# Optimization experiments

Hardware: AMD Instinct MI355X
Metric: run time of the kernel (lower is better)

The kernel has to match this reference:

```python
import jax, jax.numpy as jnp
import numpy as np

B, S, D = 8, 512, 768
H = 12          # attention heads
E = 14          # routed experts
K = 4           # top-k experts per sequence
HID = D * 2     # expert mlp hidden (mlp_ratio=2)
SH = D * 2 * 2  # shared expert hidden (mlp_ratio * n_shared_experts)
EPS = 1e-5


def _ln(x, g, b):
    m = x.mean(-1, keepdims=True)
    v = ((x - m) ** 2).mean(-1, keepdims=True)
    return (x - m) / jnp.sqrt(v + EPS) * g + b


def _gelu(x):
    return jax.nn.gelu(x, approximate=False)


def setup_inputs() -> dict:
    key = jax.random.key(0)
    ks = jax.random.split(key, 12)
    p = lambda k, shape: jax.random.normal(k, shape, jnp.float32) * 0.02
    z = lambda *shape: jnp.zeros(shape, jnp.float32)
    return {
        "x": jax.random.normal(ks[0], (B, S, D), jnp.float32),
        "ln1_g": jnp.ones((D,), jnp.float32), "ln1_b": z(D),
        "qkv_w": p(ks[1], (D, 3 * D)),
        "proj_w": p(ks[2], (D, D)), "proj_b": z(D),
        "ln2_g": jnp.ones((D,), jnp.float32), "ln2_b": z(D),
        "router_w1": p(ks[3], (D, D)), "router_b1": z(D),
        "router_w2": p(ks[4], (D, E)), "router_b2": z(E),
        "exp_w1": p(ks[5], (E, D, HID)), "exp_b1": z(E, HID),
        "exp_w2": p(ks[6], (E, HID, D)), "exp_b2": z(E, D),
        "sh_w1": p(ks[7], (D, SH)), "sh_b1": z(SH),
        "sh_w2": p(ks[8], (SH, D)), "sh_b2": z(D),
    }


def _forward(x, ln1_g, ln1_b, qkv_w, proj_w, proj_b, ln2_g, ln2_b,
             router_w1, router_b1, router_w2, router_b2,
             exp_w1, exp_b1, exp_w2, exp_b2,
             sh_w1, sh_b1, sh_w2, sh_b2):
    dh = D // H
    scale = dh ** -0.5
    # --- attention branch ---
    h1 = _ln(x, ln1_g, ln1_b)
    qkv = (h1 @ qkv_w).reshape(B, S, 3, H, dh)
    q = jnp.moveaxis(qkv[:, :, 0], 2, 1)  # [B,H,S,dh]
    k = jnp.moveaxis(qkv[:, :, 1], 2, 1)
    v = jnp.moveaxis(qkv[:, :, 2], 2, 1)
    att = jax.nn.softmax(jnp.einsum('bhqd,bhkd->bhqk', q, k) * scale, axis=-1)
    ao = jnp.einsum('bhqk,bhkd->bqhd', att, v).reshape(B, S, D) @ proj_w + proj_b
    x2 = x + ao
    # --- MoE branch ---
    h = _ln(x2, ln2_g, ln2_b)
    seq_repr = h.mean(axis=1)                                   # [B,D]
    logits = _gelu(seq_repr @ router_w1 + router_b1) @ router_w2 + router_b2  # [B,E]
    probs = jax.nn.softmax(logits, axis=-1)
    tw, ti = jax.lax.top_k(probs, K)                            # [B,K]
    tw = jax.nn.softmax(tw, axis=-1)                            # re-normalize top-k
    w = (jax.nn.one_hot(ti, E, dtype=tw.dtype) * tw[..., None]).sum(1)  # [B,E]
    # dense all-expert compute; zero weight off the top-k replicates masked routing
    hid = _gelu(jnp.einsum('bsd,edh->ebsh', h, exp_w1) + exp_b1[:, None, None, :])
    eo = jnp.einsum('ebsh,ehd->ebsd', hid, exp_w2) + exp_b2[:, None, None, :]
    y = jnp.einsum('ebsd,be->bsd', eo, w)
    # shared experts
    y = y + _gelu(h @ sh_w1 + sh_b1) @ sh_w2 + sh_b2
    return x2 + y  # ls2 is Identity (init_values=None); aux_loss=0 in eval


def reference(x, ln1_g, ln1_b, qkv_w, proj_w, proj_b, ln2_g, ln2_b,
              router_w1, router_b1, router_w2, router_b2,
              exp_w1, exp_b1, exp_w2, exp_b2,
              sh_w1, sh_b1, sh_w2, sh_b2):
    return _forward(x, ln1_g, ln1_b, qkv_w, proj_w, proj_b, ln2_g, ln2_b,
                    router_w1, router_b1, router_w2, router_b2,
                    exp_w1, exp_b1, exp_w2, exp_b2,
                    sh_w1, sh_b1, sh_w2, sh_b2)
```

## Files before the change

### kernel.cpp

```cpp
#include <hip/hip_runtime.h>
#include <hip/hip_bf16.h>


typedef _Float16 f16x8 __attribute__((ext_vector_type(8)));
typedef float f32x4 __attribute__((ext_vector_type(4)));
typedef _Float16 f16;

__device__ __forceinline__ float gelu_fast(float x) {
  const float k2l2e = 2.f * 0.7978845608028654f * 1.4426950408889634f;
  float u = (x + 0.044715f * x * x * x) * k2l2e;
  float t = exp2f(u);
  return x * (1.f - 1.f / (t + 1.f));
}

__device__ __forceinline__ f32x4 mfma16(f16x8 a, f16x8 b, f32x4 c) {
  return __builtin_amdgcn_mfma_f32_16x16x32_f16(a, b, c, 0, 0, 0);
}

#define ASYNC_CP16(g, l)                                            \
  __builtin_amdgcn_global_load_lds(                                 \
      (const __attribute__((address_space(1))) void*)(g),           \
      (__attribute__((address_space(3))) void*)(l), 16, 0, 0)

#define GEMM_STAGE(AB, WB, LDA, LDB, koff, buf)                               \
  ASYNC_CP16(&(AB)[(long)fr * (LDA) + (koff) + fc],        &sA[(buf) * 4096 + f]);        \
  ASYNC_CP16(&(AB)[(long)(fr + 64) * (LDA) + (koff) + fc], &sA[(buf) * 4096 + f + 2048]); \
  ASYNC_CP16(&(WB)[(long)fr * (LDB) + (koff) + fc],        &sB[(buf) * 4096 + f]);        \
  ASYNC_CP16(&(WB)[(long)(fr + 64) * (LDB) + (koff) + fc], &sB[(buf) * 4096 + f + 2048]);

#define GEMM_CORE(AB, WB, LDA, LDB, KK)                                       \
  {                                                                           \
    GEMM_STAGE(AB, WB, LDA, LDB, 0, 0)                                        \
    __syncthreads();                                                          \
    int cur = 0;                                                              \
    for (int k0 = 0; k0 < (KK); k0 += 32) {                                   \
      f16x8 av[4], bv[4];                                                     \
      _Pragma("unroll")                                                       \
      for (int i = 0; i < 4; i++)                                             \
        av[i] = *(const f16x8*)&sA[cur * 4096 + (wm + i * 16 + lr) * 32 + q4 * 8]; \
      _Pragma("unroll")                                                       \
      for (int j = 0; j < 4; j++)                                             \
        bv[j] = *(const f16x8*)&sB[cur * 4096 + (wn + j * 16 + lr) * 32 + q4 * 8]; \
      if (k0 + 32 < (KK)) {                                                   \
        GEMM_STAGE(AB, WB, LDA, LDB, k0 + 32, cur ^ 1)                        \
      }                                                                       \
      _Pragma("unroll")                                                       \
      for (int i = 0; i < 4; i++)                                             \
        _Pragma("unroll")                                                     \
        for (int j = 0; j < 4; j++) acc[i][j] = mfma16(av[i], bv[j], acc[i][j]); \
      if (k0 + 32 < (KK)) __syncthreads();                                    \
      cur ^= 1;                                                               \
    }                                                                         \
  }

__global__ __launch_bounds__(256) void ln_kernel(
    const float* __restrict__ x, const float* __restrict__ g,
    const float* __restrict__ bt, f16* __restrict__ out,
    float* __restrict__ mout, float* __restrict__ rout)
{
  const int row = blockIdx.x;
  const float* xr = x + (long)row * 768;
  const int t = threadIdx.x;
  float v0 = xr[t], v1 = xr[t + 256], v2 = xr[t + 512];
  __shared__ float sb[8];
  float s = v0 + v1 + v2;
  #pragma unroll
  for (int o = 32; o > 0; o >>= 1) s += __shfl_xor(s, o, 64);
  const int w = t >> 6;
  if ((t & 63) == 0) sb[w] = s;
  __syncthreads();
  const float mean = (sb[0] + sb[1] + sb[2] + sb[3]) * (1.0f / 768.0f);
  const float d0 = v0 - mean, d1 = v1 - mean, d2 = v2 - mean;
  float q = d0 * d0 + d1 * d1 + d2 * d2;
  #pragma unroll
  for (int o = 32; o > 0; o >>= 1) q += __shfl_xor(q, o, 64);
  if ((t & 63) == 0) sb[4 + w] = q;
  __syncthreads();
  const float var = (sb[4] + sb[5] + sb[6] + sb[7]) * (1.0f / 768.0f);
  const float rstd = rsqrtf(var + 1e-5f);
  f16* orow = out + (long)row * 768;
  orow[t]       = (f16)(d0 * rstd * g[t]       + bt[t]);
  orow[t + 256] = (f16)(d1 * rstd * g[t + 256] + bt[t + 256]);
  orow[t + 512] = (f16)(d2 * rstd * g[t + 512] + bt[t + 512]);
  if (t == 0) { mout[row] = mean; rout[row] = rstd; }
}

struct TransArgs {
  const float* src[6];
  f16* dst[6];
  int rows[6], cols[6];
  int start[7];
};

__global__ __launch_bounds__(256) void transpose_all(TransArgs ta) {
  const int bid = blockIdx.x;
  int m = 0;
  #pragma unroll
  for (int i = 1; i < 6; i++) if (bid >= ta.start[i]) m = i;
  const int rows = ta.rows[m], cols = ta.cols[m];
  const int tilesC = cols >> 5;
  const int perB = (rows >> 5) * tilesC;
  int local = bid - ta.start[m];
  const int z = local / perB; local -= z * perB;
  const int tr = local / tilesC, tc = local - tr * tilesC;
  const float* inb = ta.src[m] + (long)z * rows * cols;
  f16* outb = ta.dst[m] + (long)z * rows * cols;
  const int c0 = tc * 32, r0 = tr * 32;
  __shared__ float tile[32][33];
  const int tx = threadIdx.x & 31, ty = threadIdx.x >> 5;
  #pragma unroll
  for (int i = 0; i < 32; i += 8)
    tile[ty + i][tx] = inb[(long)(r0 + ty + i) * cols + c0 + tx];
  __syncthreads();
  #pragma unroll
  for (int i = 0; i < 32; i += 8)
    outb[(long)(c0 + ty + i) * rows + r0 + tx] = (f16)tile[tx][ty + i];
}

#define EPI_QKV     0
#define EPI_RESID   1

template <int EPI>
__global__ __launch_bounds__(256) void gemm_bt(
    const f16* __restrict__ A, int K, long strideA, int aShift,
    const f16* __restrict__ W, long strideW,
    const float* __restrict__ bias, int strideBias,
    const int* __restrict__ topkIdx,
    void* __restrict__ outv, long strideOut, int ldout,
    const float* __restrict__ resid)
{
  __shared__ f16 sA[2 * 128 * 32];
  __shared__ f16 sB[2 * 128 * 32];
  const int tid = threadIdx.x;
  const int pair = blockIdx.z;
  const int m0 = blockIdx.y * 128;
  const int n0 = blockIdx.x * 128;
  const f16* Ab = A + ((long)(pair >> aShift)) * strideA + (long)m0 * K;
  const int wsel = topkIdx ? topkIdx[pair] : pair;
  const f16* Wb = W + (long)wsel * strideW + (long)n0 * K;

  const int f = tid * 8;
  const int fr = f >> 5;
  const int fc = f & 31;
  const int lane = tid & 63, wid = tid >> 6;
  const int wm = (wid >> 1) * 64, wn = (wid & 1) * 64;
  const int lr = lane & 15, q4 = lane >> 4;

  f32x4 zero = {0.f, 0.f, 0.f, 0.f};
  f32x4 acc[4][4];
  #pragma unroll
  for (int i = 0; i < 4; i++)
    #pragma unroll
    for (int j = 0; j < 4; j++) acc[i][j] = zero;

  GEMM_CORE(Ab, Wb, K, K, K);

  #pragma unroll
  for (int i = 0; i < 4; i++) {
    #pragma unroll
    for (int j = 0; j < 4; j++) {
      #pragma unroll
      for (int r = 0; r < 4; r++) {
        const int row = m0 + wm + i * 16 + q4 * 4 + r;
        const int col = n0 + wn + j * 16 + lr;
        float v = acc[i][j][r];
        if constexpr (EPI == EPI_QKV) {
          f16* qb = (f16*)outv;
          const int i3 = col / 768;
          const int rem = col - i3 * 768;
          const int hh = rem >> 6, dd = rem & 63;
          const int bb = row >> 9, ss = row & 511;
          const long bh = bb * 12 + hh;
          if (i3 == 0)      qb[(bh * 512 + ss) * 64 + dd] = (f16)v;
          else if (i3 == 1) qb[3145728 + (bh * 512 + ss) * 64 + dd] = (f16)v;
          else              qb[6291456 + (bh * 64 + dd) * 512 + ss] = (f16)v;
        } else {
          float* ob = (float*)outv;
          v += bias[col];
          ob[(long)row * ldout + col] = resid[(long)row * ldout + col] + v;
        }
      }
    }
  }
}

__global__ __launch_bounds__(256) void gemm_ffn1(
    const f16* __restrict__ hbuf,
    const f16* __restrict__ shw1t, const float* __restrict__ shb1,
    const f16* __restrict__ ew1t,  const float* __restrict__ eb1,
    const int* __restrict__ topk,  const float* __restrict__ wslot,
    f16* __restrict__ shid, f16* __restrict__ hid)
{
  __shared__ f16 sA[2 * 128 * 32];
  __shared__ f16 sB[2 * 128 * 32];
  const int orig = blockIdx.x;
  const int xcd = orig & 7, slot = orig >> 3;

  const int tid = threadIdx.x;
  const int f = tid * 8;
  const int fr = f >> 5, fc = f & 31;
  const int lane = tid & 63, wid = tid >> 6;
  const int wm = (wid >> 1) * 64, wn = (wid & 1) * 64;
  const int lr = lane & 15, q4 = lane >> 4;

  const f16* Ab;
  const f16* Wb;
  const float* bp;
  f16* outp;
  int ldo;
  float wscale;

  if (slot < 96) {
    const int l = xcd * 96 + slot;
    const int bx = l % 24, by = l / 24;
    const int n0 = bx * 128, m0 = by * 128;
    Ab = hbuf + (long)m0 * 768;
    Wb = shw1t + (long)n0 * 768;
    bp = shb1 + n0;
    outp = shid + (long)m0 * 3072 + n0;
    ldo = 3072;
    wscale = 1.f;
  } else {
    const int l = xcd * 192 + (slot - 96);
    const int bx = l % 12;
    const int u = l / 12;
    const int by = u & 3, pair = u >> 2;
    const int wsel = topk[pair];
    const int n0 = bx * 128;
    const int m0g = (pair >> 2) * 512 + by * 128;
    Ab = hbuf + (long)m0g * 768;
    Wb = ew1t + (long)wsel * (1536L * 768) + (long)n0 * 768;
    bp = eb1 + (long)wsel * 1536 + n0;
    outp = hid + (long)pair * (512L * 1536) + (long)(by * 128) * 1536 + n0;
    ldo = 1536;
    wscale = wslot[pair];
  }

  f32x4 zero = {0.f, 0.f, 0.f, 0.f};
  f32x4 acc[4][4];
  #pragma unroll
  for (int i = 0; i < 4; i++)
    #pragma unroll
    for (int j = 0; j < 4; j++) acc[i][j] = zero;

  GEMM_CORE(Ab, Wb, 768, 768, 768);

  #pragma unroll
  for (int i = 0; i < 4; i++)
    #pragma unroll
    for (int j = 0; j < 4; j++)
      #pragma unroll
      for (int r = 0; r < 4; r++) {
        const int rr = wm + i * 16 + q4 * 4 + r;
        const int cc = wn + j * 16 + lr;
        float v = acc[i][j][r] + bp[cc];
        outp[(long)rr * ldo + cc] = (f16)(gelu_fast(v) * wscale);
      }
}

__global__ __launch_bounds__(256) void gemm_ffn2(
    const f16* __restrict__ shid, const f16* __restrict__ shw2t,
    const float* __restrict__ shb2, const float* __restrict__ x2,
    const f16* __restrict__ hid, const f16* __restrict__ ew2t,
    const float* __restrict__ eb2,
    const int* __restrict__ topk, const float* __restrict__ wslot,
    float* __restrict__ dout, f16* __restrict__ eo)
{
  __shared__ f16 sA[2 * 128 * 32];
  __shared__ f16 sB[2 * 128 * 32];
  const int orig = blockIdx.x;
  const int xcd = orig & 7, slot = orig >> 3;

  const int tid = threadIdx.x;
  const int f = tid * 8;
  const int fr = f >> 5, fc = f & 31;
  const int lane = tid & 63, wid = tid >> 6;
  const int wm = (wid >> 1) * 64, wn = (wid & 1) * 64;
  const int lr = lane & 15, q4 = lane >> 4;

  const bool shared_role = (slot < 24);
  const f16* Ab;
  const f16* Wb;
  int K, m0, n0, pair = 0, wsel = 0;

  if (shared_role) {
    const int l = xcd * 24 + slot;
    const int bx = l % 6, by = l / 6;
    n0 = bx * 128; m0 = by * 128;
    K = 3072;
    Ab = shid + (long)m0 * 3072;
    Wb = shw2t + (long)n0 * 3072;
  } else {
    const int l = xcd * 96 + (slot - 24);
    const int bx = l % 6;
    const int u = l / 6;
    const int by = u & 3; pair = u >> 2;
    wsel = topk[pair];
    n0 = bx * 128; m0 = by * 128;
    K = 1536;
    Ab = hid + (long)pair * (512L * 1536) + (long)m0 * 1536;
    Wb = ew2t + (long)wsel * (768L * 1536) + (long)n0 * 1536;
  }

  f32x4 zero = {0.f, 0.f, 0.f, 0.f};
  f32x4 acc[4][4];
  #pragma unroll
  for (int i = 0; i < 4; i++)
    #pragma unroll
    for (int j = 0; j < 4; j++) acc[i][j] = zero;

  if (shared_role) {
    GEMM_CORE(Ab, Wb, 3072, 3072, 3072);
  } else {
    GEMM_CORE(Ab, Wb, 1536, 1536, 1536);
  }

  if (shared_role) {
    float* op = dout + (long)m0 * 768 + n0;
    const float* rp = x2 + (long)m0 * 768 + n0;
    const float* bp = shb2 + n0;
    #pragma unroll
    for (int i = 0; i < 4; i++)
      #pragma unroll
      for (int j = 0; j < 4; j++)
        #pragma unroll
        for (int r = 0; r < 4; r++) {
          const int rr = wm + i * 16 + q4 * 4 + r;
          const int cc = wn + j * 16 + lr;
          op[(long)rr * 768 + cc] = rp[(long)rr * 768 + cc] + acc[i][j][r] + bp[cc];
        }
  } else {
    const float wscale = wslot[pair];
    f16* op = eo + (long)pair * (512L * 768) + (long)m0 * 768 + n0;
    const float* bp = eb2 + (long)wsel * 768 + n0;
    #pragma unroll
    for (int i = 0; i < 4; i++)
      #pragma unroll
      for (int j = 0; j < 4; j++)
        #pragma unroll
        for (int r = 0; r < 4; r++) {
          const int rr = wm + i * 16 + q4 * 4 + r;
          const int cc = wn + j * 16 + lr;
          op[(long)rr * 768 + cc] = (f16)(acc[i][j][r] + wscale * bp[cc]);
        }
  }
}

__device__ __forceinline__ int pswz(int row, int col) {
  return row * 512 + (col ^ ((row & 7) << 3));
}

__global__ __launch_bounds__(256) void attn_kernel(
    const f16* __restrict__ Q, const f16* __restrict__ Kt,
    const f16* __restrict__ Vt, f16* __restrict__ AO)
{
  __shared__ f16 Ps[64 * 512];
  const int bh = blockIdx.x;
  const int qt = blockIdx.y;
  const int t = threadIdx.x;
  const int lane = t & 63, w = t >> 6;
  const int lr = lane & 15, q4 = lane >> 4;
  const int r0 = qt * 64 + w * 16;
  const int lrow0 = w * 16;
  const f16* Qh = Q + (long)bh * 512 * 64;
  const f16* Kh = Kt + (long)bh * 512 * 64;

  f32x4 zero = {0.f, 0.f, 0.f, 0.f};
  f32x4 acc[32];
  #pragma unroll
  for (int i = 0; i < 32; i++) acc[i] = zero;

  #pragma unroll
  for (int kk = 0; kk < 2; kk++) {
    f16x8 a = *(const f16x8*)&Qh[(r0 + lr) * 64 + kk * 32 + q4 * 8];
    #pragma unroll
    for (int nt = 0; nt < 32; nt++) {
      f16x8 b = *(const f16x8*)&Kh[(nt * 16 + lr) * 64 + kk * 32 + q4 * 8];
      acc[nt] = mfma16(a, b, acc[nt]);
    }
  }

  const float cscale = 0.125f * 1.44269504089f;
  #pragma unroll
  for (int r = 0; r < 4; r++) {
    float m = -1e30f;
    #pragma unroll
    for (int nt = 0; nt < 32; nt++) m = fmaxf(m, acc[nt][r]);
    #pragma unroll
    for (int o = 1; o < 16; o <<= 1) m = fmaxf(m, __shfl_xor(m, o, 64));
    float s = 0.f;
    #pragma unroll
    for (int nt = 0; nt < 32; nt++) {
      float e = exp2f((acc[nt][r] - m) * cscale);
      acc[nt][r] = e; s += e;
    }
    #pragma unroll
    for (int o = 1; o < 16; o <<= 1) s += __shfl_xor(s, o, 64);
    const float inv = 1.f / s;
    const int lrow = lrow0 + q4 * 4 + r;
    #pragma unroll
    for (int nt = 0; nt < 32; nt++)
      Ps[pswz(lrow, nt * 16 + lr)] = (f16)(acc[nt][r] * inv);
  }

  const f16* Vh = Vt + (long)bh * 64 * 512;
  f32x4 o4[4];
  #pragma unroll
  for (int i = 0; i < 4; i++) o4[i] = zero;
  #pragma unroll
  for (int kk = 0; kk < 16; kk++) {
    f16x8 a = *(const f16x8*)&Ps[pswz(lrow0 + lr, kk * 32 + q4 * 8)];
    #pragma unroll
    for (int nt = 0; nt < 4; nt++) {
      f16x8 b = *(const f16x8*)&Vh[(nt * 16 + lr) * 512 + kk * 32 + q4 * 8];
      o4[nt] = mfma16(a, b, o4[nt]);
    }
  }
  const int b_ = bh / 12, h_ = bh - b_ * 12;
  #pragma unroll
  for (int nt = 0; nt < 4; nt++)
    #pragma unroll
    for (int r = 0; r < 4; r++) {
      const int rowg = r0 + q4 * 4 + r;
      AO[((long)(b_ * 512 + rowg)) * 768 + h_ * 64 + nt * 16 + lr] = (f16)o4[nt][r];
    }
}

__global__ __launch_bounds__(256) void router_reduce(
    const float* __restrict__ x2, const float* __restrict__ lnm,
    const float* __restrict__ lnr, float* __restrict__ part)
{
  const int c = blockIdx.x, b = blockIdx.y, t = threadIdx.x;
  float a0 = 0.f, a1 = 0.f, a2 = 0.f;
  #pragma unroll 4
  for (int s = 0; s < 32; s++) {
    const long base = (long)b * 512 + c * 32 + s;
    const float m = lnm[base], r = lnr[base];
    const float* xr = x2 + base * 768;
    a0 += (xr[t] - m) * r;
    a1 += (xr[t + 256] - m) * r;
    a2 += (xr[t + 512] - m) * r;
  }
  float* pr = part + ((long)b * 16 + c) * 768;
  pr[t] = a0; pr[t + 256] = a1; pr[t + 512] = a2;
}

__global__ __launch_bounds__(256) void router_seq(
    const float* __restrict__ part, const float* __restrict__ g2,
    const float* __restrict__ b2ln, float* __restrict__ seqg)
{
  const int b = blockIdx.x, t = threadIdx.x;
  const float* pb = part + (long)b * 16 * 768;
  #pragma unroll
  for (int i = 0; i < 3; i++) {
    const int j = t + 256 * i;
    float a = 0.f;
    #pragma unroll
    for (int c = 0; c < 16; c++) a += pb[c * 768 + j];
    seqg[b * 768 + j] = a * (1.f / 512.f) * g2[j] + b2ln[j];
  }
}

__global__ __launch_bounds__(256) void router_mlp1(
    const float* __restrict__ seqg, const float* __restrict__ rw1,
    float* __restrict__ pmlp)
{
  const int c = blockIdx.x, b = blockIdx.y, t = threadIdx.x;
  const float* sq = seqg + b * 768 + c * 48;
  float a0 = 0.f, a1 = 0.f, a2 = 0.f;
  #pragma unroll 8
  for (int d = 0; d < 48; d++) {
    const float s = sq[d];
    const float* wr = rw1 + (long)(c * 48 + d) * 768;
    a0 += s * wr[t];
    a1 += s * wr[t + 256];
    a2 += s * wr[t + 512];
  }
  float* pr = pmlp + ((long)b * 16 + c) * 768;
  pr[t] = a0; pr[t + 256] = a1; pr[t + 512] = a2;
}

__global__ __launch_bounds__(256) void router_fold(
    const float* __restrict__ pmlp, const float* __restrict__ rb1,
    float* __restrict__ g1g)
{
  const int b = blockIdx.x, t = threadIdx.x;
  const float* pb = pmlp + (long)b * 16 * 768;
  #pragma unroll
  for (int i = 0; i < 3; i++) {
    const int j = t + 256 * i;
    float a = rb1[j];
    #pragma unroll
    for (int c = 0; c < 16; c++) a += pb[c * 768 + j];
    g1g[b * 768 + j] = 0.5f * a * (1.0f + erff(a * 0.70710678118654752f));
  }
}

__global__ __launch_bounds__(256) void router_top(
    const float* __restrict__ g1g, const float* __restrict__ rw2,
    const float* __restrict__ rb2, float* __restrict__ wslot,
    int* __restrict__ topkIdx)
{
  __shared__ float lg[14];
  const int b = blockIdx.x, t = threadIdx.x;
  const int e = t >> 4, sub = t & 15;
  if (e < 14) {
    float a = 0.f;
    #pragma unroll
    for (int i = 0; i < 48; i++) {
      const int d = sub + 16 * i;
      a += g1g[b * 768 + d] * rw2[d * 14 + e];
    }
    #pragma unroll
    for (int o = 1; o < 16; o <<= 1) a += __shfl_xor(a, o, 64);
    if (sub == 0) lg[e] = a + rb2[e];
  }
  __syncthreads();
  if (t == 0) {
    float mx = -1e30f;
    for (int ee = 0; ee < 14; ee++) mx = fmaxf(mx, lg[ee]);
    float p[14], s = 0.f;
    for (int ee = 0; ee < 14; ee++) { p[ee] = expf(lg[ee] - mx); s += p[ee]; }
    for (int ee = 0; ee < 14; ee++) p[ee] /= s;
    int idx[4]; float val[4]; bool used[14];
    for (int ee = 0; ee < 14; ee++) used[ee] = false;
    for (int k = 0; k < 4; k++) {
      int best = -1; float bv = -1.f;
      for (int ee = 0; ee < 14; ee++)
        if (!used[ee] && p[ee] > bv) { bv = p[ee]; best = ee; }
      used[best] = true; idx[k] = best; val[k] = bv;
    }
    const float m2 = val[0];
    float ss = 0.f, e4[4];
    for (int k = 0; k < 4; k++) { e4[k] = expf(val[k] - m2); ss += e4[k]; }
    for (int k = 0; k < 4; k++) {
      wslot[b * 4 + k] = e4[k] / ss;
      topkIdx[b * 4 + k] = idx[k];
    }
  }
}

__global__ __launch_bounds__(256) void combine_kernel(
    const f16* __restrict__ eo, float* __restrict__ out)
{
  const long i = (long)blockIdx.x * 256 + threadIdx.x;
  const long b = i / (512L * 768);
  const long loc = i - b * (512L * 768);
  const f16* e0 = eo + b * 4 * (512L * 768) + loc;
  float v = out[i];
  v += (float)e0[0] + (float)e0[512L * 768] + (float)e0[2 * 512L * 768] +
       (float)e0[3 * 512L * 768];
  out[i] = v;
}

static const long OFF_X2    = 0L;
static const long OFF_LNM   = 12582912L;
static const long OFF_LNR   = OFF_LNM + 16384L;
static const long OFF_WSLOT = OFF_LNR + 16384L;
static const long OFF_TOPK  = OFF_WSLOT + 256L;
static const long OFF_PART  = OFF_TOPK + 256L;
static const long OFF_SEQG  = OFF_PART + 393216L;
static const long OFF_PMLP  = OFF_SEQG + 24576L;
static const long OFF_G1G   = OFF_PMLP + 393216L;
static const long W_QKVWT  = 13631488L;
static const long W_PROJWT = W_QKVWT + 3538944L;
static const long W_EW1T   = W_PROJWT + 1179648L;
static const long W_EW2T   = W_EW1T + 33030144L;
static const long W_SHW1T  = W_EW2T + 33030144L;
static const long W_SHW2T  = W_SHW1T + 4718592L;
static const long OFF_ACT  = 93847552L;
static const long A_H1     = OFF_ACT;
static const long A_Q      = OFF_ACT + 6291456L;
static const long A_AO     = A_Q + 18874368L;
static const long B_H      = OFF_ACT;
static const long B_HID    = OFF_ACT + 6291456L;
static const long B_SHID   = B_HID + 50331648L;
static const long B_EO     = B_SHID + 25165824L;

extern "C" void kernel_launch(void* const* d_in, const int* in_sizes, int n_in,
                              void* d_out, int out_size, void* d_ws, size_t ws_size,
                              hipStream_t stream) {
  const float* x     = (const float*)d_in[0];
  const float* ln1g  = (const float*)d_in[1];
  const float* ln1b  = (const float*)d_in[2];
  const float* qkvw  = (const float*)d_in[3];
  const float* projw = (const float*)d_in[4];
  const float* projb = (const float*)d_in[5];
  const float* ln2g  = (const float*)d_in[6];
  const float* ln2b  = (const float*)d_in[7];
  const float* rw1   = (const float*)d_in[8];
  const float* rb1   = (const float*)d_in[9];
  const float* rw2   = (const float*)d_in[10];
  const float* rb2   = (const float*)d_in[11];
  const float* ew1   = (const float*)d_in[12];
  const float* eb1   = (const float*)d_in[13];
  const float* ew2   = (const float*)d_in[14];
  const float* eb2   = (const float*)d_in[15];
  const float* shw1  = (const float*)d_in[16];
  const float* shb1  = (const float*)d_in[17];
  const float* shw2  = (const float*)d_in[18];
  const float* shb2  = (const float*)d_in[19];

  char* ws = (char*)d_ws;
  float* x2    = (float*)(ws + OFF_X2);
  float* lnm   = (float*)(ws + OFF_LNM);
  float* lnr   = (float*)(ws + OFF_LNR);
  float* wslot = (float*)(ws + OFF_WSLOT);
  int*   topk  = (int*)(ws + OFF_TOPK);
  float* part  = (float*)(ws + OFF_PART);
  float* seqg  = (float*)(ws + OFF_SEQG);
  float* pmlp  = (float*)(ws + OFF_PMLP);
  float* g1g   = (float*)(ws + OFF_G1G);
  f16* qkvwt  = (f16*)(ws + W_QKVWT);
  f16* projwt = (f16*)(ws + W_PROJWT);
  f16* ew1t   = (f16*)(ws + W_EW1T);
  f16* ew2t   = (f16*)(ws + W_EW2T);
  f16* shw1t  = (f16*)(ws + W_SHW1T);
  f16* shw2t  = (f16*)(ws + W_SHW2T);
  f16* h1     = (f16*)(ws + A_H1);
  f16* Qb     = (f16*)(ws + A_Q);
  f16* aob    = (f16*)(ws + A_AO);
  f16* hbuf   = (f16*)(ws + B_H);
  f16* hid    = (f16*)(ws + B_HID);
  f16* shid   = (f16*)(ws + B_SHID);
  f16* eo     = (f16*)(ws + B_EO);

  TransArgs ta;
  ta.src[0] = qkvw;  ta.dst[0] = qkvwt;  ta.rows[0] = 768;  ta.cols[0] = 2304;
  ta.src[1] = projw; ta.dst[1] = projwt; ta.rows[1] = 768;  ta.cols[1] = 768;
  ta.src[2] = ew1;   ta.dst[2] = ew1t;   ta.rows[2] = 768;  ta.cols[2] = 1536;
  ta.src[3] = ew2;   ta.dst[3] = ew2t;   ta.rows[3] = 1536; ta.cols[3] = 768;
  ta.src[4] = shw1;  ta.dst[4] = shw1t;  ta.rows[4] = 768;  ta.cols[4] = 3072;
  ta.src[5] = shw2;  ta.dst[5] = shw2t;  ta.rows[5] = 3072; ta.cols[5] = 768;
  ta.start[0] = 0;     ta.start[1] = 1728;  ta.start[2] = 2304;
  ta.start[3] = 18432; ta.start[4] = 34560; ta.start[5] = 36864;
  ta.start[6] = 39168;
  transpose_all<<<39168, 256, 0, stream>>>(ta);

  ln_kernel<<<4096, 256, 0, stream>>>(x, ln1g, ln1b, h1, lnm, lnr);
  gemm_bt<EPI_QKV><<<dim3(18, 32, 1), 256, 0, stream>>>(
      h1, 768, 0, 0, qkvwt, 0, nullptr, 0, nullptr, (void*)Qb, 0, 0, nullptr);
  attn_kernel<<<dim3(96, 8, 1), 256, 0, stream>>>(Qb, Qb + 3145728, Qb + 6291456, aob);
  gemm_bt<EPI_RESID><<<dim3(6, 32, 1), 256, 0, stream>>>(
      aob, 768, 0, 0, projwt, 0, projb, 0, nullptr, (void*)x2, 0, 768, x);

  ln_kernel<<<4096, 256, 0, stream>>>(x2, ln2g, ln2b, hbuf, lnm, lnr);
  router_reduce<<<dim3(16, 8, 1), 256, 0, stream>>>(x2, lnm, lnr, part);
  router_seq<<<8, 256, 0, stream>>>(part, ln2g, ln2b, seqg);
  router_mlp1<<<dim3(16, 8, 1), 256, 0, stream>>>(seqg, rw1, pmlp);
  router_fold<<<8, 256, 0, stream>>>(pmlp, rb1, g1g);
  router_top<<<8, 256, 0, stream>>>(g1g, rw2, rb2, wslot, topk);
  gemm_ffn1<<<2304, 256, 0, stream>>>(hbuf, shw1t, shb1, ew1t, eb1,
                                      topk, wslot, shid, hid);
  gemm_ffn2<<<960, 256, 0, stream>>>(shid, shw2t, shb2, x2, hid, ew2t, eb2,
                                     topk, wslot, (float*)d_out, eo);
  combine_kernel<<<12288, 256, 0, stream>>>(eo, (float*)d_out);
}
```

Before: 588.2 us.

## Triple-buffer FFN1 GEMM, stage epilogues through LDS, vectorize combine

gemm_ffn1 moves to a three-stage LDS ring that uses explicit vmcnt waits and a single barrier per k-step, so global-to-LDS loads run two tiles ahead of the MFMAs. The FFN1 and FFN2 epilogues now write results into LDS and then store 16-byte vectors to global memory, replacing scattered 2-byte and 4-byte stores. The combine kernel handles four elements per thread using f32x4 and f16x4 loads. This raises LDS use in ffn1 to 48KB, which may lower occupancy, and it relies on hand-counted vmcnt values being correct.

```diff
diff --git a/kernel.cpp b/kernel.cpp
--- a/kernel.cpp
+++ b/kernel.cpp
@@ -3,6 +3,7 @@
 
 
 typedef _Float16 f16x8 __attribute__((ext_vector_type(8)));
+typedef _Float16 f16x4 __attribute__((ext_vector_type(4)));
 typedef float f32x4 __attribute__((ext_vector_type(4)));
 typedef _Float16 f16;
 
@@ -28,7 +29,7 @@
   ASYNC_CP16(&(WB)[(long)fr * (LDB) + (koff) + fc],        &sB[(buf) * 4096 + f]);        \
   ASYNC_CP16(&(WB)[(long)(fr + 64) * (LDB) + (koff) + fc], &sB[(buf) * 4096 + f + 2048]);
 
-#define GEMM_CORE(AB, WB, LDA, LDB, KK)                                       \
+#define GEMM_CORE2(AB, WB, LDA, LDB, KK)                                      \
   {                                                                           \
     GEMM_STAGE(AB, WB, LDA, LDB, 0, 0)                                        \
     __syncthreads();                                                          \
@@ -53,6 +54,39 @@
     }                                                                         \
   }
 
+#define GEMM_CORE3(AB, WB, LDA, LDB, KK)                                      \
+  {                                                                           \
+    GEMM_STAGE(AB, WB, LDA, LDB, 0, 0)                                        \
+    GEMM_STAGE(AB, WB, LDA, LDB, 32, 1)                                       \
+    int cur = 0;                                                              \
+    for (int k0 = 0; k0 < (KK); k0 += 32) {                                   \
+      if (k0 + 32 < (KK)) {                                                   \
+        asm volatile("s_waitcnt vmcnt(4)" ::: "memory");                      \
+      } else {                                                                \
+        asm volatile("s_waitcnt vmcnt(0)" ::: "memory");                      \
+      }                                                                       \
+      __builtin_amdgcn_s_barrier();                                           \
+      __builtin_amdgcn_sched_barrier(0);                                      \
+      if (k0 + 64 < (KK)) {                                                   \
+        const int nb = (cur + 2 >= 3) ? cur - 1 : cur + 2;                    \
+        GEMM_STAGE(AB, WB, LDA, LDB, k0 + 64, nb)                             \
+      }                                                                       \
+      f16x8 av[4], bv[4];                                                     \
+      _Pragma("unroll")                                                       \
+      for (int i = 0; i < 4; i++)                                             \
+        av[i] = *(const f16x8*)&sA[cur * 4096 + (wm + i * 16 + lr) * 32 + q4 * 8]; \
+      _Pragma("unroll")                                                       \
+      for (int j = 0; j < 4; j++)                                             \
+        bv[j] = *(const f16x8*)&sB[cur * 4096 + (wn + j * 16 + lr) * 32 + q4 * 8]; \
+      _Pragma("unroll")                                                       \
+      for (int i = 0; i < 4; i++)                                             \
+        _Pragma("unroll")                                                     \
+        for (int j = 0; j < 4; j++) acc[i][j] = mfma16(av[i], bv[j], acc[i][j]); \
+      __builtin_amdgcn_sched_barrier(0x38F);                                  \
+      cur = (cur == 2) ? 0 : cur + 1;                                         \
+    }                                                                         \
+  }
+
 __global__ __launch_bounds__(256) void ln_kernel(
     const float* __restrict__ x, const float* __restrict__ g,
     const float* __restrict__ bt, f16* __restrict__ out,
@@ -153,7 +187,7 @@
     #pragma unroll
     for (int j = 0; j < 4; j++) acc[i][j] = zero;
 
-  GEMM_CORE(Ab, Wb, K, K, K);
+  GEMM_CORE2(Ab, Wb, K, K, K);
 
   #pragma unroll
   for (int i = 0; i < 4; i++) {
@@ -191,8 +225,9 @@
     const int* __restrict__ topk,  const float* __restrict__ wslot,
     f16* __restrict__ shid, f16* __restrict__ hid)
 {
-  __shared__ f16 sA[2 * 128 * 32];
-  __shared__ f16 sB[2 * 128 * 32];
+  __shared__ f16 smem[3 * 4096 * 2];
+  f16* sA = smem;
+  f16* sB = smem + 3 * 4096;
   const int orig = blockIdx.x;
   const int xcd = orig & 7, slot = orig >> 3;
 
@@ -243,8 +278,9 @@
     #pragma unroll
     for (int j = 0; j < 4; j++) acc[i][j] = zero;
 
-  GEMM_CORE(Ab, Wb, 768, 768, 768);
-
+  GEMM_CORE3(Ab, Wb, 768, 768, 768);
+
+  __syncthreads();
   #pragma unroll
   for (int i = 0; i < 4; i++)
     #pragma unroll
@@ -254,8 +290,19 @@
         const int rr = wm + i * 16 + q4 * 4 + r;
         const int cc = wn + j * 16 + lr;
         float v = acc[i][j][r] + bp[cc];
-        outp[(long)rr * ldo + cc] = (f16)(gelu_fast(v) * wscale);
+        smem[rr * 128 + cc] = (f16)(gelu_fast(v) * wscale);
       }
+  __syncthreads();
+  {
+    const int rsub = tid >> 4;
+    const int cseg = (tid & 15) * 8;
+    #pragma unroll
+    for (int g = 0; g < 8; g++) {
+      const int row = g * 16 + rsub;
+      *(f16x8*)&outp[(long)row * ldo + cseg] =
+          *(const f16x8*)&smem[row * 128 + cseg];
+    }
+  }
 }
 
 __global__ __launch_bounds__(256) void gemm_ffn2(
@@ -266,8 +313,9 @@
     const int* __restrict__ topk, const float* __restrict__ wslot,
     float* __restrict__ dout, f16* __restrict__ eo)
 {
-  __shared__ f16 sA[2 * 128 * 32];
-  __shared__ f16 sB[2 * 128 * 32];
+  __shared__ f16 smem[2 * 4096 * 2];
+  f16* sA = smem;
+  f16* sB = smem + 2 * 4096;
   const int orig = blockIdx.x;
   const int xcd = orig & 7, slot = orig >> 3;
 
@@ -281,13 +329,12 @@
   const bool shared_role = (slot < 24);
   const f16* Ab;
   const f16* Wb;
-  int K, m0, n0, pair = 0, wsel = 0;
+  int m0, n0, pair = 0, wsel = 0;
 
   if (shared_role) {
     const int l = xcd * 24 + slot;
     const int bx = l % 6, by = l / 6;
     n0 = bx * 128; m0 = by * 128;
-    K = 3072;
     Ab = shid + (long)m0 * 3072;
     Wb = shw2t + (long)n0 * 3072;
   } else {
@@ -297,7 +344,6 @@
     const int by = u & 3; pair = u >> 2;
     wsel = topk[pair];
     n0 = bx * 128; m0 = by * 128;
-    K = 1536;
     Ab = hid + (long)pair * (512L * 1536) + (long)m0 * 1536;
     Wb = ew2t + (long)wsel * (768L * 1536) + (long)n0 * 1536;
   }
@@ -310,15 +356,46 @@
     for (int j = 0; j < 4; j++) acc[i][j] = zero;
 
   if (shared_role) {
-    GEMM_CORE(Ab, Wb, 3072, 3072, 3072);
+    GEMM_CORE2(Ab, Wb, 3072, 3072, 3072);
   } else {
-    GEMM_CORE(Ab, Wb, 1536, 1536, 1536);
-  }
-
+    GEMM_CORE2(Ab, Wb, 1536, 1536, 1536);
+  }
+
+  __syncthreads();
   if (shared_role) {
+    float* sf = (float*)smem;
     float* op = dout + (long)m0 * 768 + n0;
     const float* rp = x2 + (long)m0 * 768 + n0;
     const float* bp = shb2 + n0;
+    #pragma unroll
+    for (int p = 0; p < 2; p++) {
+      if ((wid >> 1) == p) {
+        #pragma unroll
+        for (int i = 0; i < 4; i++)
+          #pragma unroll
+          for (int j = 0; j < 4; j++)
+            #pragma unroll
+            for (int r = 0; r < 4; r++)
+              sf[(i * 16 + q4 * 4 + r) * 128 + wn + j * 16 + lr] = acc[i][j][r];
+      }
+      __syncthreads();
+      #pragma unroll
+      for (int g = 0; g < 8; g++) {
+        const int rl = g * 8 + (tid >> 5);
+        const int c4 = (tid & 31) * 4;
+        const int grow = p * 64 + rl;
+        f32x4 v = *(const f32x4*)&sf[rl * 128 + c4];
+        const f32x4 rv = *(const f32x4*)&rp[(long)grow * 768 + c4];
+        const f32x4 bv = *(const f32x4*)&bp[c4];
+        v = v + rv + bv;
+        *(f32x4*)&op[(long)grow * 768 + c4] = v;
+      }
+      __syncthreads();
+    }
+  } else {
+    const float wscale = wslot[pair];
+    const float* bp = eb2 + (long)wsel * 768 + n0;
+    f16* op = eo + (long)pair * (512L * 768) + (long)m0 * 768 + n0;
     #pragma unroll
     for (int i = 0; i < 4; i++)
       #pragma unroll
@@ -327,22 +404,17 @@
         for (int r = 0; r < 4; r++) {
           const int rr = wm + i * 16 + q4 * 4 + r;
           const int cc = wn + j * 16 + lr;
-          op[(long)rr * 768 + cc] = rp[(long)rr * 768 + cc] + acc[i][j][r] + bp[cc];
+          smem[rr * 128 + cc] = (f16)(acc[i][j][r] + wscale * bp[cc]);
         }
-  } else {
-    const float wscale = wslot[pair];
-    f16* op = eo + (long)pair * (512L * 768) + (long)m0 * 768 + n0;
-    const float* bp = eb2 + (long)wsel * 768 + n0;
-    #pragma unroll
-    for (int i = 0; i < 4; i++)
-      #pragma unroll
-      for (int j = 0; j < 4; j++)
-        #pragma unroll
-        for (int r = 0; r < 4; r++) {
-          const int rr = wm + i * 16 + q4 * 4 + r;
-          const int cc = wn + j * 16 + lr;
-          op[(long)rr * 768 + cc] = (f16)(acc[i][j][r] + wscale * bp[cc]);
-        }
+    __syncthreads();
+    const int rsub = tid >> 4;
+    const int cseg = (tid & 15) * 8;
+    #pragma unroll
+    for (int g = 0; g < 8; g++) {
+      const int row = g * 16 + rsub;
+      *(f16x8*)&op[(long)row * 768 + cseg] =
+          *(const f16x8*)&smem[row * 128 + cseg];
+    }
   }
 }
 
@@ -543,14 +615,20 @@
 __global__ __launch_bounds__(256) void combine_kernel(
     const f16* __restrict__ eo, float* __restrict__ out)
 {
-  const long i = (long)blockIdx.x * 256 + threadIdx.x;
-  const long b = i / (512L * 768);
-  const long loc = i - b * (512L * 768);
+  const long i4 = ((long)blockIdx.x * 256 + threadIdx.x) * 4;
+  const long b = i4 / (512L * 768);
+  const long loc = i4 - b * (512L * 768);
   const f16* e0 = eo + b * 4 * (512L * 768) + loc;
-  float v = out[i];
-  v += (float)e0[0] + (float)e0[512L * 768] + (float)e0[2 * 512L * 768] +
-       (float)e0[3 * 512L * 768];
-  out[i] = v;
+  f32x4 v = *(const f32x4*)&out[i4];
+  #pragma unroll
+  for (int s = 0; s < 4; s++) {
+    const f16x4 ev = *(const f16x4*)&e0[s * (512L * 768)];
+    v.x += (float)ev[0];
+    v.y += (float)ev[1];
+    v.z += (float)ev[2];
+    v.w += (float)ev[3];
+  }
+  *(f32x4*)&out[i4] = v;
 }
 
 static const long OFF_X2    = 0L;
@@ -654,5 +732,5 @@
                                       topk, wslot, shid, hid);
   gemm_ffn2<<<960, 256, 0, stream>>>(shid, shw2t, shb2, x2, hid, ew2t, eb2,
                                      topk, wslot, (float*)d_out, eo);
-  combine_kernel<<<12288, 256, 0, stream>>>(eo, (float*)d_out);
-}
+  combine_kernel<<<3072, 256, 0, stream>>>(eo, (float*)d_out);
+}
```

Measured after the change: 583.9 us. Within noise of the previous version (-0.7%).
